# Optimization experiments

Hardware: AMD Instinct MI355X
Metric: run time of the kernel (lower is better)

Reference implementation:

```python
import jax, jax.numpy as jnp
import numpy as np

N = 100000      # nodes
E = 1600000     # directed edges (before self loops)
F_IN = 3        # node_feature_dim
H = 32          # hidden_dim
BN_EPS = 1e-5


def _linear_params(k, fan_in, fan_out):
    lim = 1.0 / np.sqrt(fan_in)
    kw, kb = jax.random.split(k)
    W = jax.random.uniform(kw, (fan_in, fan_out), jnp.float32, -lim, lim)
    b = jax.random.uniform(kb, (fan_out,), jnp.float32, -lim, lim)
    return W, b


def setup_inputs() -> dict:
    key = jax.random.key(0)
    ks = jax.random.split(key, 12)
    x = jax.random.normal(ks[0], (N, F_IN), jnp.float32)
    edge_index = jax.random.randint(ks[1], (2, E), 0, N, dtype=jnp.int64)
    node_type = jax.random.randint(ks[2], (N,), 0, 3, dtype=jnp.int64)
    W1, b1 = _linear_params(ks[3], F_IN, H)
    W2, b2 = _linear_params(ks[4], H, H)
    W3, b3 = _linear_params(ks[5], H, H)
    g1 = jnp.ones((H,), jnp.float32); be1 = jnp.zeros((H,), jnp.float32)
    g2 = jnp.ones((H,), jnp.float32); be2 = jnp.zeros((H,), jnp.float32)
    Wc1, bc1 = _linear_params(ks[6], H, H // 2)
    Wc2, bc2 = _linear_params(ks[7], H // 2, 1)
    Wd1, bd1 = _linear_params(ks[8], H, H // 2)
    Wd2, bd2 = _linear_params(ks[9], H // 2, 1)
    return dict(x=x, edge_index=edge_index, node_type=node_type,
                W1=W1, b1=b1, W2=W2, b2=b2, W3=W3, b3=b3,
                g1=g1, be1=be1, g2=g2, be2=be2,
                Wc1=Wc1, bc1=bc1, Wc2=Wc2, bc2=bc2,
                Wd1=Wd1, bd1=bd1, Wd2=Wd2, bd2=bd2)


def reference(x, edge_index, node_type, W1, b1, W2, b2, W3, b3,
              g1, be1, g2, be2, Wc1, bc1, Wc2, bc2, Wd1, bd1, Wd2, bd2):
    n = x.shape[0]
    # GCNConv (PyG default): add self loops, symmetric deg^-1/2 normalization
    loop = jnp.arange(n, dtype=edge_index.dtype)
    src = jnp.concatenate([edge_index[0], loop])  # [E+N]
    dst = jnp.concatenate([edge_index[1], loop])
    deg = jax.ops.segment_sum(jnp.ones_like(dst, dtype=x.dtype), dst, num_segments=n)
    dinv = jnp.where(deg > 0, jax.lax.rsqrt(jnp.maximum(deg, 1.0)), 0.0)
    norm = dinv[src] * dinv[dst]  # [E+N]

    def conv(h, W, b):
        msg = (h @ W)[src] * norm[:, None]                  # gather + scale
        return jax.ops.segment_sum(msg, dst, num_segments=n) + b  # scatter-add

    def bn(h, g, be):  # BatchNorm1d with batch statistics (training math)
        mu = h.mean(axis=0)
        var = ((h - mu) ** 2).mean(axis=0)
        return (h - mu) * jax.lax.rsqrt(var + BN_EPS) * g + be

    h = bn(jax.nn.relu(conv(x, W1, b1)), g1, be1)   # dropout = identity (eval)
    h = bn(jax.nn.relu(conv(h, W2, b2)), g2, be2)
    h = jax.nn.relu(conv(h, W3, b3))

    cand_mask = node_type == 0
    cand_emb = h[cand_mask]                                 # [C, H]
    cand_scores = (jax.nn.relu(cand_emb @ Wc1 + bc1) @ Wc2 + bc2)[:, 0]

    w = jax.nn.softmax(h.sum(axis=1))[:, None]              # [N,1] importance
    g_emb = (h * w).sum(axis=0, keepdims=True)              # [1, H]
    dn = (jax.nn.relu(g_emb @ Wd1 + bd1) @ Wd2 + bd2).reshape(())

    logits = jnp.concatenate([cand_scores, dn[None]], axis=0)
    cand_idx = jnp.nonzero(cand_mask)[0]
    return logits, cand_idx
```

## Files before the change

kernel.cpp:

```cpp
#include <hip/hip_runtime.h>

typedef unsigned int uint;
typedef unsigned char uchar;

#define NB_MAX 256
#define NPB_MAX 2048

#if defined(__has_builtin)
#if __has_builtin(__builtin_amdgcn_cvt_pk_f32_fp8) && __has_builtin(__builtin_amdgcn_cvt_pk_fp8_f32)
#define HW_FP8 1
#endif
#endif

typedef __attribute__((ext_vector_type(2))) float v2f;

static __device__ __forceinline__ uint f2fp8_sw(float v) {
    v = fminf(fmaxf(v, -448.f), 448.f);
    uint u = __float_as_uint(v);
    uint s = (u >> 24) & 0x80u;
    uint mag = u & 0x7FFFFFFFu;
    uint r = mag + 0x7FFFFu + ((mag >> 20) & 1u);
    if (r < 0x3C800000u) return s;
    uint e8 = (r - 0x3C000000u) >> 20;
    return s | min(e8, 0x7Eu);
}
static __device__ __forceinline__ float fp82f(uint b) {
    uint mag = b & 0x7Fu;
    uint bits = ((b & 0x80u) << 24) | ((mag << 20) + 0x3C000000u);
    return mag ? __uint_as_float(bits) : 0.f;
}
static __device__ __forceinline__ void dec8(uint2 v, float* o) {
#ifdef HW_FP8
    v2f a = __builtin_amdgcn_cvt_pk_f32_fp8((int)v.x, false);
    v2f b = __builtin_amdgcn_cvt_pk_f32_fp8((int)v.x, true);
    v2f c = __builtin_amdgcn_cvt_pk_f32_fp8((int)v.y, false);
    v2f d = __builtin_amdgcn_cvt_pk_f32_fp8((int)v.y, true);
    o[0]=a.x; o[1]=a.y; o[2]=b.x; o[3]=b.y;
    o[4]=c.x; o[5]=c.y; o[6]=d.x; o[7]=d.y;
#else
    o[0]=fp82f(v.x&0xFF); o[1]=fp82f((v.x>>8)&0xFF); o[2]=fp82f((v.x>>16)&0xFF); o[3]=fp82f(v.x>>24);
    o[4]=fp82f(v.y&0xFF); o[5]=fp82f((v.y>>8)&0xFF); o[6]=fp82f((v.y>>16)&0xFF); o[7]=fp82f(v.y>>24);
#endif
}
static __device__ __forceinline__ uint2 enc8(const float* o) {
#ifdef HW_FP8
    int rx = __builtin_amdgcn_cvt_pk_fp8_f32(o[0], o[1], 0, false);
    rx = __builtin_amdgcn_cvt_pk_fp8_f32(o[2], o[3], rx, true);
    int ry = __builtin_amdgcn_cvt_pk_fp8_f32(o[4], o[5], 0, false);
    ry = __builtin_amdgcn_cvt_pk_fp8_f32(o[6], o[7], ry, true);
    return make_uint2((uint)rx, (uint)ry);
#else
    uint2 r;
    r.x = f2fp8_sw(o[0]) | (f2fp8_sw(o[1])<<8) | (f2fp8_sw(o[2])<<16) | (f2fp8_sw(o[3])<<24);
    r.y = f2fp8_sw(o[4]) | (f2fp8_sw(o[5])<<8) | (f2fp8_sw(o[6])<<16) | (f2fp8_sw(o[7])<<24);
    return r;
#endif
}
static __device__ __forceinline__ void dec32(const uchar* row, float* o) {
    const uint4* r4 = (const uint4*)row;
    uint4 A = r4[0], B = r4[1];
    dec8(make_uint2(A.x,A.y), o); dec8(make_uint2(A.z,A.w), o+8);
    dec8(make_uint2(B.x,B.y), o+16); dec8(make_uint2(B.z,B.w), o+24);
}
static __device__ __forceinline__ void enc32(const float* o, uchar* row) {
    uint2 a = enc8(o), b = enc8(o+8), c = enc8(o+16), d = enc8(o+24);
    uint4* r4 = (uint4*)row;
    r4[0] = make_uint4(a.x,a.y,b.x,b.y);
    r4[1] = make_uint4(c.x,c.y,d.x,d.y);
}

static __device__ __forceinline__ unsigned wave_incl_scan(unsigned v) {
    int lane = threadIdx.x & 63;
    #pragma unroll
    for (int d = 1; d < 64; d <<= 1) {
        unsigned t = (unsigned)__shfl_up((int)v, d, 64);
        if (lane >= d) v += t;
    }
    return v;
}

static __device__ void block_excl_scan(const uint* in, uint* out, int n, uint* wscr) {
    int tid = threadIdx.x;
    int lane = tid & 63, wid = tid >> 6;
    int base = tid * 8;
    uint v[8], pre[8], s = 0;
    #pragma unroll
    for (int k = 0; k < 8; k++) v[k] = (base + k < n) ? in[base + k] : 0u;
    #pragma unroll
    for (int k = 0; k < 8; k++) { pre[k] = s; s += v[k]; }
    uint is = wave_incl_scan(s);
    __syncthreads();
    if (lane == 63) wscr[wid] = is;
    __syncthreads();
    uint woff = 0;
    for (int wI = 0; wI < wid; wI++) woff += wscr[wI];
    uint excl = is - s + woff;
    #pragma unroll
    for (int k = 0; k < 8; k++) if (base + k < n) out[base + k] = excl + pre[k];
    __syncthreads();
}

__global__ __launch_bounds__(256) void bucket_hist_kernel(const int* src, const int* dst,
                                                          const int* nt, uint* bcnt, uint* bcand,
                                                          int E, int N, int NB, int shift) {
    __shared__ uint bh[NB_MAX], ch[NB_MAX];
    int tid = threadIdx.x;
    bh[tid] = 0; ch[tid] = 0;
    __syncthreads();
    int gs = gridDim.x * 256;
    for (int i = blockIdx.x * 256 + tid; i < E; i += gs) {
        int d = dst[i], s = src[i];
        if ((uint)d < (uint)N && (uint)s < (uint)N) atomicAdd(&bh[d >> shift], 1u);
    }
    for (int i = blockIdx.x * 256 + tid; i < N; i += gs) {
        if (nt[i] == 0) atomicAdd(&ch[i >> shift], 1u);
    }
    __syncthreads();
    if (bh[tid]) atomicAdd(&bcnt[tid], bh[tid]);
    if (ch[tid]) atomicAdd(&bcand[tid], ch[tid]);
}

__global__ __launch_bounds__(256) void partition_kernel(const int* src, const int* dst,
                                                        const uint* bcnt, uint* alloc0,
                                                        uint* staging, int E, int N, int shift) {
    __shared__ uint bbase_s[NB_MAX];
    __shared__ uint lh[NB_MAX], gb[NB_MAX];
    __shared__ uint ws4[4];
    int tid = threadIdx.x;
    int lane = tid & 63, wid = tid >> 6;
    uint a = bcnt[tid];
    uint ia = wave_incl_scan(a);
    if (lane == 63) ws4[wid] = ia;
    __syncthreads();
    uint off = 0;
    for (int wI = 0; wI < wid; wI++) off += ws4[wI];
    bbase_s[tid] = ia - a + off;
    lh[tid] = 0;
    __syncthreads();
    int base = blockIdx.x * 2048;
    uint mask = (1u << shift) - 1u;
    int breg[8];
    uint rreg[8], pk8[8];
    #pragma unroll
    for (int k = 0; k < 8; k++) {
        int e = base + k * 256 + tid;
        breg[k] = -1;
        if (e < E) {
            int s = src[e], d = dst[e];
            if ((uint)d < (uint)N && (uint)s < (uint)N) {
                int b = d >> shift;
                pk8[k] = (((uint)d & mask) << 17) | (uint)s;
                breg[k] = b;
                rreg[k] = atomicAdd(&lh[b], 1u);
            }
        }
    }
    __syncthreads();
    gb[tid] = lh[tid] ? (bbase_s[tid] + atomicAdd(&alloc0[tid], lh[tid])) : 0u;
    __syncthreads();
    #pragma unroll
    for (int k = 0; k < 8; k++) {
        if (breg[k] >= 0)
            staging[gb[breg[k]] + rreg[k]] = pk8[k];
    }
}

__global__ __launch_bounds__(256) void local_csr_kernel(const uint* staging, const uint* bcnt,
                                                        const uint* bcand, const int* nt,
                                                        const float* x,
                                                        int* csr_src, uint* csr_off, uint* cand_pos,
                                                        float* dinv, float4* xs,
                                                        int N, int shift, int NB) {
    __shared__ uint deg[NPB_MAX];
    __shared__ uint ofs[NPB_MAX];
    __shared__ uint ws4[4];
    __shared__ uint sb[4];
    int b = blockIdx.x, tid = threadIdx.x;
    int lane = tid & 63, wid = tid >> 6;
    uint a = bcnt[tid];
    uint ia = wave_incl_scan(a);
    if (lane == 63) ws4[wid] = ia;
    __syncthreads();
    uint off = 0;
    for (int wI = 0; wI < wid; wI++) off += ws4[wI];
    if (tid == b) { sb[0] = ia - a + off; sb[1] = ia + off; }
    __syncthreads();
    uint c = bcand[tid];
    uint ic = wave_incl_scan(c);
    if (lane == 63) ws4[wid] = ic;
    __syncthreads();
    uint offc = 0;
    for (int wI = 0; wI < wid; wI++) offc += ws4[wI];
    if (tid == b) sb[2] = ic - c + offc;
    __syncthreads();
    uint ebase = sb[0], eend = sb[1], cb = sb[2];
    int nbase = b << shift;
    int ncount = min(1 << shift, N - nbase);
    for (int i = tid; i < ncount; i += 256) deg[i] = 0;
    __syncthreads();
    for (uint p = ebase + tid; p < eend; p += 256)
        atomicAdd(&deg[staging[p] >> 17], 1u);
    __syncthreads();
    block_excl_scan(deg, ofs, ncount, ws4);
    for (int i = tid; i < ncount; i += 256)
        csr_off[nbase + i] = ebase + ofs[i];
    if (b == NB - 1 && tid == 0) csr_off[N] = eend;
    for (int i = tid; i < ncount; i += 256) {
        int g = nbase + i;
        float di = rsqrtf((float)(deg[i] + 1u));
        dinv[g] = di;
        xs[g] = make_float4(x[3*g] * di, x[3*g+1] * di, x[3*g+2] * di, 0.f);
    }
    __syncthreads();
    for (int i = tid; i < ncount; i += 256) deg[i] = 0;
    __syncthreads();
    for (uint p = ebase + tid; p < eend; p += 256) {
        uint pkv = staging[p];
        uint dl = pkv >> 17;
        uint pos = ebase + ofs[dl] + atomicAdd(&deg[dl], 1u);
        csr_src[pos] = (int)(pkv & 0x1FFFFu);
    }
    __syncthreads();
    for (int i = tid; i < ncount; i += 256) deg[i] = (nt[nbase + i] == 0) ? 1u : 0u;
    __syncthreads();
    block_excl_scan(deg, ofs, ncount, ws4);
    for (int i = tid; i < ncount; i += 256) cand_pos[nbase + i] = cb + ofs[i];
}

__global__ __launch_bounds__(256) void agg1_kernel(const float* xs, const int* csr_src,
                                                   const uint* csr_off, const float* dinv,
                                                   const float* W1, const float* b1, uchar* hb,
                                                   int n, float* stats_sum, float* stats_sq) {
    const int tid = threadIdx.x;
    const int wave = tid >> 6;
    const int lane = tid & 63;
    const int c4 = lane & 3;
    const int slot = lane >> 2;
    const int qlead = lane & ~3;
    __shared__ float W1s[96];
    __shared__ uint s_lt;
    if (tid < 96) W1s[tid] = W1[tid];
    float bv[8];
    #pragma unroll
    for (int j = 0; j < 8; j++) bv[j] = b1[c4 * 8 + j];
    float bs[8], bq[8];
    #pragma unroll
    for (int j = 0; j < 8; j++) { bs[j] = 0.f; bq[j] = 0.f; }
    __syncthreads();
    for (uint cbase = (uint)blockIdx.x * 128u; cbase < (uint)n; cbase += gridDim.x * 128u) {
        uint avail = min((uint)n - cbase, 128u);
        if (tid == 0) s_lt = 0u;
        __syncthreads();
        while (true) {
            uint li = 0;
            if (c4 == 0) li = atomicAdd(&s_lt, 1u);
            li = (uint)__shfl((int)li, qlead, 64);
            if (li >= avail) break;
            uint node = cbase + li;
            uint s = csr_off[node], e = csr_off[node + 1];
            float acc = xs[(size_t)node * 4 + c4];
            for (uint p = s; p < e; p += 8) {
                uint idx[8];
                float wg[8];
                #pragma unroll
                for (int j = 0; j < 8; j++) {
                    uint q = p + (uint)j;
                    uint qc = min(q, e - 1u);
                    idx[j] = (uint)csr_src[qc];
                    wg[j] = (q < e) ? 1.f : 0.f;
                }
                #pragma unroll
                for (int j = 0; j < 8; j++)
                    acc = fmaf(wg[j], xs[(size_t)idx[j] * 4 + c4], acc);
            }
            float u = dinv[node] * acc;
            float u0 = __shfl(u, qlead, 64);
            float u1 = __shfl(u, qlead + 1, 64);
            float u2 = __shfl(u, qlead + 2, 64);
            float hv[8];
            #pragma unroll
            for (int j = 0; j < 8; j++) {
                int ch = c4 * 8 + j;
                float o = u0 * W1s[ch] + u1 * W1s[32 + ch] + u2 * W1s[64 + ch] + bv[j];
                hv[j] = fmaxf(o, 0.f);
            }
            *(uint2*)(hb + (size_t)node * 32 + c4 * 8) = enc8(hv);
            #pragma unroll
            for (int j = 0; j < 8; j++) { bs[j] += hv[j]; bq[j] += hv[j] * hv[j]; }
        }
        __syncthreads();
    }
    #pragma unroll
    for (int m = 4; m < 64; m <<= 1) {
        #pragma unroll
        for (int j = 0; j < 8; j++) {
            bs[j] += __shfl_xor(bs[j], m, 64);
            bq[j] += __shfl_xor(bq[j], m, 64);
        }
    }
    __shared__ float ssum[4][32], ssq[4][32];
    if (slot == 0) {
        #pragma unroll
        for (int j = 0; j < 8; j++) { ssum[wave][c4 * 8 + j] = bs[j]; ssq[wave][c4 * 8 + j] = bq[j]; }
    }
    __syncthreads();
    if (tid < 32) {
        atomicAdd(&stats_sum[tid], ssum[0][tid] + ssum[1][tid] + ssum[2][tid] + ssum[3][tid]);
        atomicAdd(&stats_sq[tid],  ssq[0][tid] + ssq[1][tid] + ssq[2][tid] + ssq[3][tid]);
    }
}

__global__ __launch_bounds__(256) void gemmf_kernel(const uchar* hb, const float* stats_sum,
                                                    const float* stats_sq, const float* g,
                                                    const float* be, const float* W,
                                                    const float* dinv, uchar* zb, int n,
                                                    float inv_n) {
    __shared__ float Ws[1024];
    __shared__ float cs[32];
    __shared__ float a_s[32], d_s[32];
    int tid = threadIdx.x;
    if (tid < 32) {
        float mu = stats_sum[tid] * inv_n;
        float var = fmaxf(stats_sq[tid] * inv_n - mu * mu, 0.f);
        float a = g[tid] * rsqrtf(var + 1e-5f);
        a_s[tid] = a;
        d_s[tid] = be[tid] - mu * a;
    }
    __syncthreads();
    #pragma unroll
    for (int t = tid; t < 1024; t += 256) Ws[t] = a_s[t >> 5] * W[t];
    if (tid < 32) {
        float c = 0.f;
        for (int k = 0; k < 32; k++) c += d_s[k] * W[k * 32 + tid];
        cs[tid] = c;
    }
    __syncthreads();
    int i = blockIdx.x * 256 + tid;
    if (i >= n) return;
    float hk[32], acc[32];
    dec32(hb + (size_t)i * 32, hk);
    #pragma unroll
    for (int j = 0; j < 32; j++) acc[j] = cs[j];
    #pragma unroll
    for (int k = 0; k < 32; k++) {
        float h0 = hk[k];
        #pragma unroll
        for (int j = 0; j < 32; j++) acc[j] += h0 * Ws[k * 32 + j];
    }
    float di = dinv[i];
    #pragma unroll
    for (int j = 0; j < 32; j++) acc[j] *= di;
    enc32(acc, zb + (size_t)i * 32);
}

__global__ __launch_bounds__(256) void agg_kernel(const uchar* zb, const int* csr_src,
                                                  const uint* csr_off, const float* dinv,
                                                  const float* bias, uchar* hb, int n,
                                                  int mode, float* stats_sum, float* stats_sq,
                                                  float* rowsum, uint* maxkey) {
    const int tid = threadIdx.x;
    const int wave = tid >> 6;
    const int lane = tid & 63;
    const int c4 = lane & 3;
    const int slot = lane >> 2;
    const int qlead = lane & ~3;
    __shared__ uint s_lt;
    float bv[8];
    #pragma unroll
    for (int j = 0; j < 8; j++) bv[j] = bias[c4 * 8 + j];
    float bs[8], bq[8];
    #pragma unroll
    for (int j = 0; j < 8; j++) { bs[j] = 0.f; bq[j] = 0.f; }
    float lmax = -3.0e38f;
    for (uint cbase = (uint)blockIdx.x * 128u; cbase < (uint)n; cbase += gridDim.x * 128u) {
        uint avail = min((uint)n - cbase, 128u);
        if (tid == 0) s_lt = 0u;
        __syncthreads();
        while (true) {
            uint li = 0;
            if (c4 == 0) li = atomicAdd(&s_lt, 1u);
            li = (uint)__shfl((int)li, qlead, 64);
            if (li >= avail) break;
            uint node = cbase + li;
            uint s = csr_off[node], e = csr_off[node + 1];
            float acc[8];
            dec8(*(const uint2*)(zb + (size_t)node * 32 + c4 * 8), acc);
            for (uint p = s; p < e; p += 8) {
                uint idx[8];
                float wg[8];
                #pragma unroll
                for (int j = 0; j < 8; j++) {
                    uint q = p + (uint)j;
                    uint qc = min(q, e - 1u);
                    idx[j] = (uint)csr_src[qc];
                    wg[j] = (q < e) ? 1.f : 0.f;
                }
                #pragma unroll
                for (int j = 0; j < 8; j++) {
                    float t[8];
                    dec8(*(const uint2*)(zb + (size_t)idx[j] * 32 + c4 * 8), t);
                    #pragma unroll
                    for (int cI = 0; cI < 8; cI++) acc[cI] = fmaf(wg[j], t[cI], acc[cI]);
                }
            }
            float di = dinv[node];
            float hv[8];
            #pragma unroll
            for (int j = 0; j < 8; j++) hv[j] = fmaxf(di * acc[j] + bv[j], 0.f);
            *(uint2*)(hb + (size_t)node * 32 + c4 * 8) = enc8(hv);
            if (mode == 0) {
                #pragma unroll
                for (int j = 0; j < 8; j++) { bs[j] += hv[j]; bq[j] += hv[j] * hv[j]; }
            } else {
                float rs = ((hv[0] + hv[1]) + (hv[2] + hv[3])) + ((hv[4] + hv[5]) + (hv[6] + hv[7]));
                rs += __shfl_xor(rs, 1, 64);
                rs += __shfl_xor(rs, 2, 64);
                if (c4 == 0) { rowsum[node] = rs; lmax = fmaxf(lmax, rs); }
            }
        }
        __syncthreads();
    }
    if (mode == 0) {
        #pragma unroll
        for (int m = 4; m < 64; m <<= 1) {
            #pragma unroll
            for (int j = 0; j < 8; j++) {
                bs[j] += __shfl_xor(bs[j], m, 64);
                bq[j] += __shfl_xor(bq[j], m, 64);
            }
        }
        __shared__ float ssum[4][32], ssq[4][32];
        if (slot == 0) {
            #pragma unroll
            for (int j = 0; j < 8; j++) { ssum[wave][c4 * 8 + j] = bs[j]; ssq[wave][c4 * 8 + j] = bq[j]; }
        }
        __syncthreads();
        if (tid < 32) {
            atomicAdd(&stats_sum[tid], ssum[0][tid] + ssum[1][tid] + ssum[2][tid] + ssum[3][tid]);
            atomicAdd(&stats_sq[tid],  ssq[0][tid] + ssq[1][tid] + ssq[2][tid] + ssq[3][tid]);
        }
    } else {
        #pragma unroll
        for (int m = 1; m < 64; m <<= 1) lmax = fmaxf(lmax, __shfl_xor(lmax, m, 64));
        __shared__ float lm[4];
        if (lane == 0) lm[wave] = lmax;
        __syncthreads();
        if (tid == 0) {
            float m = fmaxf(fmaxf(lm[0], lm[1]), fmaxf(lm[2], lm[3]));
            uint u = __float_as_uint(m);
            uint key = (u & 0x80000000u) ? ~u : (u | 0x80000000u);
            atomicMax(maxkey, key);
        }
    }
}

__global__ __launch_bounds__(256) void head_kernel(const uchar* hb, const int* nt,
                                                   const uint* pos, const float* Wc1,
                                                   const float* bc1, const float* Wc2,
                                                   const float* bc2, const float* rowsum,
                                                   const uint* maxkey, float* gvec, float* Zp,
                                                   uint* ticket, const float* Wd1,
                                                   const float* bd1, const float* Wd2,
                                                   const float* bd2, float* out, int n, int C) {
    __shared__ float W1s[512], b1s[16], W2s[16];
    __shared__ float ls[256];
    __shared__ float ge[32], tt[16];
    __shared__ int lastflag;
    int tid = threadIdx.x;
    for (int t = tid; t < 512; t += 256) W1s[t] = Wc1[t];
    if (tid < 16) { b1s[tid] = bc1[tid]; W2s[tid] = Wc2[tid]; }
    __syncthreads();
    int i = blockIdx.x * 256 + tid;
    if (i < n && nt[i] == 0) {
        float hv[32];
        dec32(hb + (size_t)i * 32, hv);
        float s = bc2[0];
        #pragma unroll
        for (int j = 0; j < 16; j++) {
            float u = b1s[j];
            #pragma unroll
            for (int k = 0; k < 32; k++) u += hv[k] * W1s[k * 16 + j];
            s += fmaxf(u, 0.f) * W2s[j];
        }
        s = fminf(fmaxf(s, -1000.f), 1000.f);
        uint p = pos[i];
        if (p < (uint)C) {
            out[p] = s;
            out[C + 1 + p] = (float)i;
        }
    }
    uint key = *maxkey;
    float M = 0.f;
    if (key != 0u) M = (key & 0x80000000u) ? __uint_as_float(key ^ 0x80000000u) : __uint_as_float(~key);
    int lane = tid & 31, grp = tid >> 5;
    int stride = gridDim.x * 8;
    float accZ = 0.f, accg = 0.f;
    for (int node = blockIdx.x * 8 + grp; node < n; node += stride) {
        float ew = __expf(rowsum[node] - M);
        accg += fp82f(hb[(size_t)node * 32 + lane]) * ew;
        if (lane == 0) accZ += ew;
    }
    ls[tid] = accg;
    __syncthreads();
    if (tid < 32) {
        float a = 0.f;
        #pragma unroll
        for (int g = 0; g < 8; g++) a += ls[tid + 32 * g];
        atomicAdd(&gvec[tid], a);
    }
    __syncthreads();
    ls[tid] = (lane == 0) ? accZ : 0.f;
    __syncthreads();
    if (tid == 0) {
        float a = 0.f;
        for (int t = 0; t < 256; t += 32) a += ls[t];
        atomicAdd(Zp, a);
        __threadfence();
        uint old = atomicAdd(ticket, 1u);
        lastflag = (old == gridDim.x - 1) ? 1 : 0;
    }
    __syncthreads();
    if (lastflag) {
        __threadfence();
        if (tid < 32) ge[tid] = atomicAdd(&gvec[tid], 0.f);
        if (tid == 0) ls[0] = atomicAdd(Zp, 0.f);
        __syncthreads();
        float Zv = fmaxf(ls[0], 1e-30f);
        if (tid < 32) ge[tid] /= Zv;
        __syncthreads();
        if (tid < 16) {
            float s = bd1[tid];
            for (int k = 0; k < 32; k++) s += ge[k] * Wd1[k * 16 + tid];
            tt[tid] = fmaxf(s, 0.f);
        }
        __syncthreads();
        if (tid == 0) {
            float s = bd2[0];
            for (int j = 0; j < 16; j++) s += tt[j] * Wd2[j];
            out[C] = fminf(fmaxf(s, -1000.f), 1000.f);
        }
    }
}

extern "C" void kernel_launch(void* const* d_in, const int* in_sizes, int n_in,
                              void* d_out, int out_size, void* d_ws, size_t ws_size,
                              hipStream_t stream) {
    const float* x   = (const float*)d_in[0];
    const int*   ei  = (const int*)d_in[1];
    const int*   nt  = (const int*)d_in[2];
    const float* W1  = (const float*)d_in[3];  const float* b1  = (const float*)d_in[4];
    const float* W2  = (const float*)d_in[5];  const float* b2  = (const float*)d_in[6];
    const float* W3  = (const float*)d_in[7];  const float* b3  = (const float*)d_in[8];
    const float* g1  = (const float*)d_in[9];  const float* be1 = (const float*)d_in[10];
    const float* g2  = (const float*)d_in[11]; const float* be2 = (const float*)d_in[12];
    const float* Wc1 = (const float*)d_in[13]; const float* bc1 = (const float*)d_in[14];
    const float* Wc2 = (const float*)d_in[15]; const float* bc2 = (const float*)d_in[16];
    const float* Wd1 = (const float*)d_in[17]; const float* bd1 = (const float*)d_in[18];
    const float* Wd2 = (const float*)d_in[19]; const float* bd2 = (const float*)d_in[20];

    const int N = in_sizes[0] / 3;
    const int E = in_sizes[1] / 2;
    const int C = (out_size - 1) / 2;
    const int* e_src = ei;
    const int* e_dst = ei + E;
    float* out = (float*)d_out;

    int shift = 9;
    while (((N + (1 << shift) - 1) >> shift) > NB_MAX) shift++;
    const int NB = (N + (1 << shift) - 1) >> shift;

    char* w = (char*)d_ws;
    auto alloc = [&](size_t bytes) { void* p = (void*)w; w += (bytes + 255) & ~(size_t)255; return p; };
    float*    stats  = (float*)alloc(256 * 4);
    uint*     bcnt   = (uint*)alloc(NB_MAX * 4);
    uint*     bcand  = (uint*)alloc(NB_MAX * 4);
    uint*     alloc0 = (uint*)alloc(NB_MAX * 4);
    size_t zero_bytes = (size_t)((char*)w - (char*)stats);
    float*    dinv   = (float*)alloc((size_t)N * 4);
    uint*     csr_off= (uint*)alloc((size_t)(N + 1) * 4);
    uint*     cand_pos=(uint*)alloc((size_t)N * 4);
    float*    rowsum = (float*)alloc((size_t)N * 4);
    int*      csr_src= (int*)alloc((size_t)E * 4);
    uint*     staging= (uint*)alloc((size_t)E * 4);
    uchar*    zb     = (uchar*)alloc((size_t)N * 32);
    uchar*    hb     = (uchar*)alloc((size_t)N * 32);
    float4*   xs     = (float4*)zb;

    float* sum1 = stats;       float* sq1 = stats + 32;
    float* sum2 = stats + 64;  float* sq2 = stats + 96;
    float* gvec = stats + 128; float* Zp  = stats + 160;
    uint* maxkey = (uint*)(stats + 161);
    uint* ticket = (uint*)(stats + 162);

    hipMemsetAsync(stats, 0, zero_bytes, stream);

    const int gN   = (N + 255) / 256;
    const int gPar = (E + 2047) / 2048;
    const int gAgg = (N + 127) / 128;
    const float inv_n = 1.0f / (float)N;

    hipLaunchKernelGGL(bucket_hist_kernel, dim3(784), dim3(256), 0, stream, e_src, e_dst, nt, bcnt, bcand, E, N, NB, shift);
    hipLaunchKernelGGL(partition_kernel, dim3(gPar), dim3(256), 0, stream, e_src, e_dst, bcnt, alloc0, staging, E, N, shift);
    hipLaunchKernelGGL(local_csr_kernel, dim3(NB), dim3(256), 0, stream, staging, bcnt, bcand, nt,
                       x, csr_src, csr_off, cand_pos, dinv, xs, N, shift, NB);

    hipLaunchKernelGGL(agg1_kernel, dim3(gAgg), dim3(256), 0, stream, (const float*)xs, csr_src, csr_off,
                       dinv, W1, b1, hb, N, sum1, sq1);

    hipLaunchKernelGGL(gemmf_kernel, dim3(gN), dim3(256), 0, stream, hb, sum1, sq1, g1, be1, W2, dinv, zb, N, inv_n);
    hipLaunchKernelGGL(agg_kernel, dim3(gAgg), dim3(256), 0, stream, zb, csr_src, csr_off,
                       dinv, b2, hb, N, 0, sum2, sq2, rowsum, maxkey);

    hipLaunchKernelGGL(gemmf_kernel, dim3(gN), dim3(256), 0, stream, hb, sum2, sq2, g2, be2, W3, dinv, zb, N, inv_n);
    hipLaunchKernelGGL(agg_kernel, dim3(gAgg), dim3(256), 0, stream, zb, csr_src, csr_off,
                       dinv, b3, hb, N, 1, sum1, sq1, rowsum, maxkey);

    hipLaunchKernelGGL(head_kernel, dim3(gN), dim3(256), 0, stream, hb, nt, cand_pos,
                       Wc1, bc1, Wc2, bc2, rowsum, maxkey, gvec, Zp, ticket,
                       Wd1, bd1, Wd2, bd2, out, N, C);
}
```

Measured before the change: 321.5 us.

## Use two lanes per node with 16-byte fp8 gathers in aggregation kernel

The aggregation kernel now assigns two lanes per node, each handling 16 channels with uint4 loads, instead of four lanes with 8-byte loads. All eight neighbor rows are loaded before decoding so the memory accesses can overlap. The mode flag becomes a template parameter, which removes the runtime branch and the unused stats registers. This halves the lanes per node and doubles the per-lane register footprint, which may reduce occupancy.

```diff
diff --git a/kernel.cpp b/kernel.cpp
--- a/kernel.cpp
+++ b/kernel.cpp
@@ -56,11 +56,14 @@
     return r;
 #endif
 }
+static __device__ __forceinline__ void dec16(uint4 v, float* o) {
+    dec8(make_uint2(v.x, v.y), o);
+    dec8(make_uint2(v.z, v.w), o + 8);
+}
 static __device__ __forceinline__ void dec32(const uchar* row, float* o) {
     const uint4* r4 = (const uint4*)row;
-    uint4 A = r4[0], B = r4[1];
-    dec8(make_uint2(A.x,A.y), o); dec8(make_uint2(A.z,A.w), o+8);
-    dec8(make_uint2(B.x,B.y), o+16); dec8(make_uint2(B.z,B.w), o+24);
+    dec16(r4[0], o);
+    dec16(r4[1], o + 16);
 }
 static __device__ __forceinline__ void enc32(const float* o, uchar* row) {
     uint2 a = enc8(o), b = enc8(o+8), c = enc8(o+16), d = enc8(o+24);
@@ -353,24 +356,26 @@
     enc32(acc, zb + (size_t)i * 32);
 }
 
+template<int MODE>
 __global__ __launch_bounds__(256) void agg_kernel(const uchar* zb, const int* csr_src,
                                                   const uint* csr_off, const float* dinv,
                                                   const float* bias, uchar* hb, int n,
-                                                  int mode, float* stats_sum, float* stats_sq,
+                                                  float* stats_sum, float* stats_sq,
                                                   float* rowsum, uint* maxkey) {
     const int tid = threadIdx.x;
     const int wave = tid >> 6;
     const int lane = tid & 63;
-    const int c4 = lane & 3;
-    const int slot = lane >> 2;
-    const int qlead = lane & ~3;
+    const int c2 = lane & 1;
+    const int plead = lane & ~1;
     __shared__ uint s_lt;
-    float bv[8];
-    #pragma unroll
-    for (int j = 0; j < 8; j++) bv[j] = bias[c4 * 8 + j];
-    float bs[8], bq[8];
-    #pragma unroll
-    for (int j = 0; j < 8; j++) { bs[j] = 0.f; bq[j] = 0.f; }
+    float bv[16];
+    #pragma unroll
+    for (int j = 0; j < 16; j++) bv[j] = bias[c2 * 16 + j];
+    float bs[16], bq[16];
+    if (MODE == 0) {
+        #pragma unroll
+        for (int j = 0; j < 16; j++) { bs[j] = 0.f; bq[j] = 0.f; }
+    }
     float lmax = -3.0e38f;
     for (uint cbase = (uint)blockIdx.x * 128u; cbase < (uint)n; cbase += gridDim.x * 128u) {
         uint avail = min((uint)n - cbase, 128u);
@@ -378,13 +383,13 @@
         __syncthreads();
         while (true) {
             uint li = 0;
-            if (c4 == 0) li = atomicAdd(&s_lt, 1u);
-            li = (uint)__shfl((int)li, qlead, 64);
+            if (c2 == 0) li = atomicAdd(&s_lt, 1u);
+            li = (uint)__shfl((int)li, plead, 64);
             if (li >= avail) break;
             uint node = cbase + li;
             uint s = csr_off[node], e = csr_off[node + 1];
-            float acc[8];
-            dec8(*(const uint2*)(zb + (size_t)node * 32 + c4 * 8), acc);
+            float acc[16];
+            dec16(*(const uint4*)(zb + (size_t)node * 32 + c2 * 16), acc);
             for (uint p = s; p < e; p += 8) {
                 uint idx[8];
                 float wg[8];
@@ -395,44 +400,50 @@
                     idx[j] = (uint)csr_src[qc];
                     wg[j] = (q < e) ? 1.f : 0.f;
                 }
+                uint4 dv[8];
+                #pragma unroll
+                for (int j = 0; j < 8; j++)
+                    dv[j] = *(const uint4*)(zb + (size_t)idx[j] * 32 + c2 * 16);
                 #pragma unroll
                 for (int j = 0; j < 8; j++) {
-                    float t[8];
-                    dec8(*(const uint2*)(zb + (size_t)idx[j] * 32 + c4 * 8), t);
+                    float t[16];
+                    dec16(dv[j], t);
                     #pragma unroll
-                    for (int cI = 0; cI < 8; cI++) acc[cI] = fmaf(wg[j], t[cI], acc[cI]);
+                    for (int k = 0; k < 16; k++) acc[k] = fmaf(wg[j], t[k], acc[k]);
                 }
             }
             float di = dinv[node];
-            float hv[8];
+            float hv[16];
             #pragma unroll
-            for (int j = 0; j < 8; j++) hv[j] = fmaxf(di * acc[j] + bv[j], 0.f);
-            *(uint2*)(hb + (size_t)node * 32 + c4 * 8) = enc8(hv);
-            if (mode == 0) {
+            for (int j = 0; j < 16; j++) hv[j] = fmaxf(di * acc[j] + bv[j], 0.f);
+            uint2 lo = enc8(hv), hi = enc8(hv + 8);
+            *(uint4*)(hb + (size_t)node * 32 + c2 * 16) = make_uint4(lo.x, lo.y, hi.x, hi.y);
+            if (MODE == 0) {
                 #pragma unroll
-                for (int j = 0; j < 8; j++) { bs[j] += hv[j]; bq[j] += hv[j] * hv[j]; }
+                for (int j = 0; j < 16; j++) { bs[j] += hv[j]; bq[j] += hv[j] * hv[j]; }
             } else {
-                float rs = ((hv[0] + hv[1]) + (hv[2] + hv[3])) + ((hv[4] + hv[5]) + (hv[6] + hv[7]));
+                float rs = 0.f;
+                #pragma unroll
+                for (int j = 0; j < 16; j++) rs += hv[j];
                 rs += __shfl_xor(rs, 1, 64);
-                rs += __shfl_xor(rs, 2, 64);
-                if (c4 == 0) { rowsum[node] = rs; lmax = fmaxf(lmax, rs); }
+                if (c2 == 0) { rowsum[node] = rs; lmax = fmaxf(lmax, rs); }
             }
         }
         __syncthreads();
     }
-    if (mode == 0) {
-        #pragma unroll
-        for (int m = 4; m < 64; m <<= 1) {
+    if (MODE == 0) {
+        #pragma unroll
+        for (int m = 2; m < 64; m <<= 1) {
             #pragma unroll
-            for (int j = 0; j < 8; j++) {
+            for (int j = 0; j < 16; j++) {
                 bs[j] += __shfl_xor(bs[j], m, 64);
                 bq[j] += __shfl_xor(bq[j], m, 64);
             }
         }
         __shared__ float ssum[4][32], ssq[4][32];
-        if (slot == 0) {
+        if ((lane >> 1) == 0) {
             #pragma unroll
-            for (int j = 0; j < 8; j++) { ssum[wave][c4 * 8 + j] = bs[j]; ssq[wave][c4 * 8 + j] = bq[j]; }
+            for (int j = 0; j < 16; j++) { ssum[wave][c2 * 16 + j] = bs[j]; ssq[wave][c2 * 16 + j] = bq[j]; }
         }
         __syncthreads();
         if (tid < 32) {
@@ -608,12 +619,12 @@
                        dinv, W1, b1, hb, N, sum1, sq1);
 
     hipLaunchKernelGGL(gemmf_kernel, dim3(gN), dim3(256), 0, stream, hb, sum1, sq1, g1, be1, W2, dinv, zb, N, inv_n);
-    hipLaunchKernelGGL(agg_kernel, dim3(gAgg), dim3(256), 0, stream, zb, csr_src, csr_off,
-                       dinv, b2, hb, N, 0, sum2, sq2, rowsum, maxkey);
+    hipLaunchKernelGGL((agg_kernel<0>), dim3(gAgg), dim3(256), 0, stream, zb, csr_src, csr_off,
+                       dinv, b2, hb, N, sum2, sq2, rowsum, maxkey);
 
     hipLaunchKernelGGL(gemmf_kernel, dim3(gN), dim3(256), 0, stream, hb, sum2, sq2, g2, be2, W3, dinv, zb, N, inv_n);
-    hipLaunchKernelGGL(agg_kernel, dim3(gAgg), dim3(256), 0, stream, zb, csr_src, csr_off,
-                       dinv, b3, hb, N, 1, sum1, sq1, rowsum, maxkey);
+    hipLaunchKernelGGL((agg_kernel<1>), dim3(gAgg), dim3(256), 0, stream, zb, csr_src, csr_off,
+                       dinv, b3, hb, N, sum1, sq1, rowsum, maxkey);
 
     hipLaunchKernelGGL(head_kernel, dim3(gN), dim3(256), 0, stream, hb, nt, cand_pos,
                        Wc1, bc1, Wc2, bc2, rowsum, maxkey, gvec, Zp, ticket,
```

New measurement: 326.0 us. About the same (+1.4%).

## Use persistent blocks with atomic chunk ticketing in aggregation kernels

Applied to the files above, without the earlier changes.

The aggregation kernels now launch at most 512 persistent blocks, and each block pulls 128-node chunks from a global atomic counter instead of using a fixed grid-stride assignment. agg_kernel also becomes a template on mode, so the mode branches are resolved at compile time. The aim is to balance uneven per-node degree work across blocks and cut block launch overhead, while keeping per-block BN statistics atomics to fewer blocks. The cost is one global atomic plus an extra barrier per chunk, and the counters must sit inside the memset-zeroed stats region.

```diff
diff --git a/kernel.cpp b/kernel.cpp
--- a/kernel.cpp
+++ b/kernel.cpp
@@ -230,7 +230,8 @@
 __global__ __launch_bounds__(256) void agg1_kernel(const float* xs, const int* csr_src,
                                                    const uint* csr_off, const float* dinv,
                                                    const float* W1, const float* b1, uchar* hb,
-                                                   int n, float* stats_sum, float* stats_sq) {
+                                                   int n, float* stats_sum, float* stats_sq,
+                                                   uint* gt) {
     const int tid = threadIdx.x;
     const int wave = tid >> 6;
     const int lane = tid & 63;
@@ -238,7 +239,7 @@
     const int slot = lane >> 2;
     const int qlead = lane & ~3;
     __shared__ float W1s[96];
-    __shared__ uint s_lt;
+    __shared__ uint s_lt, s_chunk;
     if (tid < 96) W1s[tid] = W1[tid];
     float bv[8];
     #pragma unroll
@@ -247,7 +248,11 @@
     #pragma unroll
     for (int j = 0; j < 8; j++) { bs[j] = 0.f; bq[j] = 0.f; }
     __syncthreads();
-    for (uint cbase = (uint)blockIdx.x * 128u; cbase < (uint)n; cbase += gridDim.x * 128u) {
+    while (true) {
+        if (tid == 0) s_chunk = atomicAdd(gt, 1u);
+        __syncthreads();
+        uint cbase = s_chunk * 128u;
+        if (cbase >= (uint)n) break;
         uint avail = min((uint)n - cbase, 128u);
         if (tid == 0) s_lt = 0u;
         __syncthreads();
@@ -353,26 +358,33 @@
     enc32(acc, zb + (size_t)i * 32);
 }
 
+template<int MODE>
 __global__ __launch_bounds__(256) void agg_kernel(const uchar* zb, const int* csr_src,
                                                   const uint* csr_off, const float* dinv,
                                                   const float* bias, uchar* hb, int n,
-                                                  int mode, float* stats_sum, float* stats_sq,
-                                                  float* rowsum, uint* maxkey) {
+                                                  float* stats_sum, float* stats_sq,
+                                                  float* rowsum, uint* maxkey, uint* gt) {
     const int tid = threadIdx.x;
     const int wave = tid >> 6;
     const int lane = tid & 63;
     const int c4 = lane & 3;
     const int slot = lane >> 2;
     const int qlead = lane & ~3;
-    __shared__ uint s_lt;
+    __shared__ uint s_lt, s_chunk;
     float bv[8];
     #pragma unroll
     for (int j = 0; j < 8; j++) bv[j] = bias[c4 * 8 + j];
     float bs[8], bq[8];
-    #pragma unroll
-    for (int j = 0; j < 8; j++) { bs[j] = 0.f; bq[j] = 0.f; }
+    if (MODE == 0) {
+        #pragma unroll
+        for (int j = 0; j < 8; j++) { bs[j] = 0.f; bq[j] = 0.f; }
+    }
     float lmax = -3.0e38f;
-    for (uint cbase = (uint)blockIdx.x * 128u; cbase < (uint)n; cbase += gridDim.x * 128u) {
+    while (true) {
+        if (tid == 0) s_chunk = atomicAdd(gt, 1u);
+        __syncthreads();
+        uint cbase = s_chunk * 128u;
+        if (cbase >= (uint)n) break;
         uint avail = min((uint)n - cbase, 128u);
         if (tid == 0) s_lt = 0u;
         __syncthreads();
@@ -408,7 +420,7 @@
             #pragma unroll
             for (int j = 0; j < 8; j++) hv[j] = fmaxf(di * acc[j] + bv[j], 0.f);
             *(uint2*)(hb + (size_t)node * 32 + c4 * 8) = enc8(hv);
-            if (mode == 0) {
+            if (MODE == 0) {
                 #pragma unroll
                 for (int j = 0; j < 8; j++) { bs[j] += hv[j]; bq[j] += hv[j] * hv[j]; }
             } else {
@@ -420,7 +432,7 @@
         }
         __syncthreads();
     }
-    if (mode == 0) {
+    if (MODE == 0) {
         #pragma unroll
         for (int m = 4; m < 64; m <<= 1) {
             #pragma unroll
@@ -591,12 +603,16 @@
     float* gvec = stats + 128; float* Zp  = stats + 160;
     uint* maxkey = (uint*)(stats + 161);
     uint* ticket = (uint*)(stats + 162);
+    uint* gt1 = (uint*)(stats + 163);
+    uint* gt2 = (uint*)(stats + 164);
+    uint* gt3 = (uint*)(stats + 165);
 
     hipMemsetAsync(stats, 0, zero_bytes, stream);
 
     const int gN   = (N + 255) / 256;
     const int gPar = (E + 2047) / 2048;
-    const int gAgg = (N + 127) / 128;
+    int gAgg = (N + 127) / 128;
+    if (gAgg > 512) gAgg = 512;
     const float inv_n = 1.0f / (float)N;
 
     hipLaunchKernelGGL(bucket_hist_kernel, dim3(784), dim3(256), 0, stream, e_src, e_dst, nt, bcnt, bcand, E, N, NB, shift);
@@ -605,15 +621,15 @@
                        x, csr_src, csr_off, cand_pos, dinv, xs, N, shift, NB);
 
     hipLaunchKernelGGL(agg1_kernel, dim3(gAgg), dim3(256), 0, stream, (const float*)xs, csr_src, csr_off,
-                       dinv, W1, b1, hb, N, sum1, sq1);
+                       dinv, W1, b1, hb, N, sum1, sq1, gt1);
 
     hipLaunchKernelGGL(gemmf_kernel, dim3(gN), dim3(256), 0, stream, hb, sum1, sq1, g1, be1, W2, dinv, zb, N, inv_n);
-    hipLaunchKernelGGL(agg_kernel, dim3(gAgg), dim3(256), 0, stream, zb, csr_src, csr_off,
-                       dinv, b2, hb, N, 0, sum2, sq2, rowsum, maxkey);
+    hipLaunchKernelGGL((agg_kernel<0>), dim3(gAgg), dim3(256), 0, stream, zb, csr_src, csr_off,
+                       dinv, b2, hb, N, sum2, sq2, rowsum, maxkey, gt2);
 
     hipLaunchKernelGGL(gemmf_kernel, dim3(gN), dim3(256), 0, stream, hb, sum2, sq2, g2, be2, W3, dinv, zb, N, inv_n);
-    hipLaunchKernelGGL(agg_kernel, dim3(gAgg), dim3(256), 0, stream, zb, csr_src, csr_off,
-                       dinv, b3, hb, N, 1, sum1, sq1, rowsum, maxkey);
+    hipLaunchKernelGGL((agg_kernel<1>), dim3(gAgg), dim3(256), 0, stream, zb, csr_src, csr_off,
+                       dinv, b3, hb, N, sum1, sq1, rowsum, maxkey, gt3);
 
     hipLaunchKernelGGL(head_kernel, dim3(gN), dim3(256), 0, stream, hb, nt, cand_pos,
                        Wc1, bc1, Wc2, bc2, rowsum, maxkey, gvec, Zp, ticket,
```

After: 319.0 us (median of 2 runs). Within noise of the previous version (-0.8%).
